# Optimization experiments

Hardware: AMD Instinct MI355X
Metric: run time of the kernel (lower is better)

## Reference

```python
import jax, jax.numpy as jnp
import numpy as np

N_BLOCKS = 8
HIDDEN = 256
BATCH = 4096
IN_DIM = 3 * N_BLOCKS


def setup_inputs() -> dict:
    key = jax.random.key(0)
    ks = jax.random.split(key, 32)
    s = 0.05
    d = {}
    d['x'] = jax.random.normal(ks[0], (BATCH, IN_DIM), dtype=jnp.float32)
    # per-block object encoders (stacked): in -> H, relu, H -> H, relu, H -> H
    d['o_W0'] = jax.random.normal(ks[1], (N_BLOCKS, IN_DIM, HIDDEN), dtype=jnp.float32) * s
    d['o_b0'] = jnp.zeros((N_BLOCKS, HIDDEN), jnp.float32)
    d['o_W1'] = jax.random.normal(ks[2], (N_BLOCKS, HIDDEN, HIDDEN), dtype=jnp.float32) * s
    d['o_b1'] = jnp.zeros((N_BLOCKS, HIDDEN), jnp.float32)
    d['o_W2'] = jax.random.normal(ks[3], (N_BLOCKS, HIDDEN, HIDDEN), dtype=jnp.float32) * s
    d['o_b2'] = jnp.zeros((N_BLOCKS, HIDDEN), jnp.float32)
    # clear predicate encoder: H -> H, relu, H -> H, relu, H -> 1, sigmoid
    d['c_W0'] = jax.random.normal(ks[4], (HIDDEN, HIDDEN), dtype=jnp.float32) * s
    d['c_b0'] = jnp.zeros((HIDDEN,), jnp.float32)
    d['c_W1'] = jax.random.normal(ks[5], (HIDDEN, HIDDEN), dtype=jnp.float32) * s
    d['c_b1'] = jnp.zeros((HIDDEN,), jnp.float32)
    d['c_W2'] = jax.random.normal(ks[6], (HIDDEN, 1), dtype=jnp.float32) * s
    d['c_b2'] = jnp.zeros((1,), jnp.float32)
    # ontable predicate encoder
    d['t_W0'] = jax.random.normal(ks[7], (HIDDEN, HIDDEN), dtype=jnp.float32) * s
    d['t_b0'] = jnp.zeros((HIDDEN,), jnp.float32)
    d['t_W1'] = jax.random.normal(ks[8], (HIDDEN, HIDDEN), dtype=jnp.float32) * s
    d['t_b1'] = jnp.zeros((HIDDEN,), jnp.float32)
    d['t_W2'] = jax.random.normal(ks[9], (HIDDEN, 1), dtype=jnp.float32) * s
    d['t_b2'] = jnp.zeros((1,), jnp.float32)
    # AonB predicate encoder: 2H -> H, relu, H -> H, relu, H -> 1, sigmoid
    d['a_W0'] = jax.random.normal(ks[10], (2 * HIDDEN, HIDDEN), dtype=jnp.float32) * s
    d['a_b0'] = jnp.zeros((HIDDEN,), jnp.float32)
    d['a_W1'] = jax.random.normal(ks[11], (HIDDEN, HIDDEN), dtype=jnp.float32) * s
    d['a_b1'] = jnp.zeros((HIDDEN,), jnp.float32)
    d['a_W2'] = jax.random.normal(ks[12], (HIDDEN, 1), dtype=jnp.float32) * s
    d['a_b2'] = jnp.zeros((1,), jnp.float32)
    return d


def _pred_mlp(h, W0, b0, W1, b1, W2, b2):
    h = jax.nn.relu(h @ W0 + b0)
    h = jax.nn.relu(h @ W1 + b1)
    return jax.nn.sigmoid(h @ W2 + b2)


def reference(x, o_W0, o_b0, o_W1, o_b1, o_W2, o_b2,
              c_W0, c_b0, c_W1, c_b1, c_W2, c_b2,
              t_W0, t_b0, t_W1, t_b1, t_W2, t_b2,
              a_W0, a_b0, a_W1, a_b1, a_W2, a_b2):
    B = x.shape[0]
    H = o_W0.shape[-1]
    # object encodings: (N, B, H), all N encoders batched via einsum
    h = jax.nn.relu(jnp.einsum('bd,ndh->nbh', x, o_W0) + o_b0[:, None, :])
    h = jax.nn.relu(jnp.einsum('nbh,nhk->nbk', h, o_W1) + o_b1[:, None, :])
    enc = jnp.einsum('nbh,nhk->nbk', h, o_W2) + o_b2[:, None, :]
    # clear/ontable predicates: (N, B, 1) -> (B, N)
    clear = _pred_mlp(enc, c_W0, c_b0, c_W1, c_b1, c_W2, c_b2)[..., 0].T
    table = _pred_mlp(enc, t_W0, t_b0, t_W1, t_b1, t_W2, t_b2)[..., 0].T
    # AonB over all pairs; split first layer to avoid materializing (N,N,B,2H)
    a_l = jnp.einsum('nbh,hk->nbk', enc, a_W0[:H])
    a_r = jnp.einsum('nbh,hk->nbk', enc, a_W0[H:])
    ph = jax.nn.relu(a_l[:, None] + a_r[None, :] + a_b0)  # (N, N, B, H), axis0=i(left), axis1=j(right)
    ph = jax.nn.relu(ph @ a_W1 + a_b1)
    aonb = jax.nn.sigmoid(ph @ a_W2 + a_b2)[..., 0]  # (N, N, B)
    aonb_b = jnp.transpose(aonb, (2, 0, 1))  # (B, N, N)
    # per block i: [AonB(i,0..N-1), clear(i), ontable(i)] concatenated over i
    out = jnp.concatenate([aonb_b, clear[..., None], table[..., None]], axis=2)
    return out.reshape(B, -1)
```

## Files before the change

### kernel.cpp

```cpp
#include <hip/hip_runtime.h>
#include <hip/hip_bf16.h>

#define OFF_O0   0u
#define OFF_O1   65536u
#define OFF_O2   589824u
#define OFF_C0   1114112u
#define OFF_C1   1179648u
#define OFF_T0   1245184u
#define OFF_T1   1310720u
#define OFF_AL   1376256u
#define OFF_AR   1441792u
#define OFF_A1   1507328u
#define OFF_ENC  1572864u
#define OFF_ALQ  9961472u
#define OFF_ARQ  18350080u

typedef short s8v __attribute__((ext_vector_type(8)));
typedef float f4v __attribute__((ext_vector_type(4)));

__device__ __forceinline__ unsigned short f2bf(float f) {
  unsigned u = __float_as_uint(f);
  unsigned r = (u + 0x7FFFu + ((u >> 16) & 1u)) >> 16;
  return (unsigned short)r;
}
__device__ __forceinline__ float bf2f(unsigned short h) {
  return __uint_as_float(((unsigned)h) << 16);
}

__device__ __forceinline__ void gemm_epilogue(
    f4v acc[4][4], const float* bias, int act,
    unsigned short* outb, unsigned short* gout)
{
  int lane = threadIdx.x & 63;
  int w    = threadIdx.x >> 6;
  int lr = lane & 15, kh = lane >> 4;
  if (outb) __syncthreads();
  #pragma unroll
  for (int nt = 0; nt < 4; nt++) {
    int col = w*64 + nt*16 + lr;
    float bv = bias ? bias[col] : 0.0f;
    #pragma unroll
    for (int mt = 0; mt < 4; mt++) {
      #pragma unroll
      for (int i = 0; i < 4; i++) {
        int row = mt*16 + kh*4 + i;
        float v = acc[mt][nt][i] + bv;
        if (act) v = fmaxf(v, 0.0f);
        unsigned short hh = f2bf(v);
        if (outb) {
          int bofs = (2*col) ^ ((row & 7) << 4);
          *(unsigned short*)((char*)outb + row*512 + bofs) = hh;
        }
        if (gout) gout[row*256 + col] = hh;
      }
    }
  }
  if (outb) __syncthreads();
}

__device__ __forceinline__ void gemm_core(
    const unsigned short* inb, const unsigned short* __restrict__ wt,
    f4v acc[4][4])
{
  int lane = threadIdx.x & 63;
  int w    = threadIdx.x >> 6;
  int lr = lane & 15, kh = lane >> 4;
  #pragma unroll
  for (int a = 0; a < 4; a++)
    #pragma unroll
    for (int b = 0; b < 4; b++) acc[a][b] = (f4v){0.f,0.f,0.f,0.f};
  #pragma unroll
  for (int k0 = 0; k0 < 256; k0 += 32) {
    s8v bfrag[4];
    #pragma unroll
    for (int nt = 0; nt < 4; nt++)
      bfrag[nt] = *(const s8v*)(wt + (w*64 + nt*16 + lr)*256 + k0 + kh*8);
    #pragma unroll
    for (int mt = 0; mt < 4; mt++) {
      int row = mt*16 + lr;
      int bofs = (2*k0 + kh*16) ^ ((row & 7) << 4);
      s8v afrag = *(const s8v*)((const char*)inb + row*512 + bofs);
      #pragma unroll
      for (int nt = 0; nt < 4; nt++)
        acc[mt][nt] = __builtin_amdgcn_mfma_f32_16x16x32_bf16(afrag, bfrag[nt], acc[mt][nt], 0, 0, 0);
    }
  }
}

__device__ __forceinline__ void gemm64(
    const unsigned short* inb, const unsigned short* __restrict__ wt,
    const float* bias, int act, unsigned short* outb, unsigned short* gout)
{
  f4v acc[4][4];
  gemm_core(inb, wt, acc);
  gemm_epilogue(acc, bias, act, outb, gout);
}

__device__ __forceinline__ void dot_tail(
    f4v acc[4][4], const float* __restrict__ bias,
    const float* __restrict__ w2, float b2,
    float* __restrict__ out, int m0, int offs, float* red)
{
  int lane = threadIdx.x & 63;
  int w    = threadIdx.x >> 6;
  int lr = lane & 15, kh = lane >> 4;
  float w2v[4], bv[4];
  #pragma unroll
  for (int nt = 0; nt < 4; nt++) {
    int col = w*64 + nt*16 + lr;
    w2v[nt] = w2[col];
    bv[nt]  = bias[col];
  }
  #pragma unroll
  for (int mt = 0; mt < 4; mt++) {
    #pragma unroll
    for (int i = 0; i < 4; i++) {
      float s = 0.0f;
      #pragma unroll
      for (int nt = 0; nt < 4; nt++)
        s += fmaxf(acc[mt][nt][i] + bv[nt], 0.0f) * w2v[nt];
      s += __shfl_xor(s, 1);
      s += __shfl_xor(s, 2);
      s += __shfl_xor(s, 4);
      s += __shfl_xor(s, 8);
      if (lr == 0) red[(mt*16 + kh*4 + i)*4 + w] = s;
    }
  }
  __syncthreads();
  if (threadIdx.x < 64) {
    int row = threadIdx.x;
    float s = red[row*4] + red[row*4+1] + red[row*4+2] + red[row*4+3];
    out[(m0 + row)*80 + offs] = 1.0f / (1.0f + __expf(-s - b2));
  }
}

__device__ __forceinline__ void gemm_x(
    const unsigned short* xb, const unsigned short* __restrict__ wt,
    const float* bias, unsigned short* outb)
{
  int lane = threadIdx.x & 63;
  int w    = threadIdx.x >> 6;
  int lr = lane & 15, kh = lane >> 4;
  f4v acc[4][4];
  #pragma unroll
  for (int a = 0; a < 4; a++)
    #pragma unroll
    for (int b = 0; b < 4; b++) acc[a][b] = (f4v){0.f,0.f,0.f,0.f};

  s8v bfrag[4];
  #pragma unroll
  for (int nt = 0; nt < 4; nt++)
    bfrag[nt] = *(const s8v*)(wt + (w*64 + nt*16 + lr)*32 + kh*8);
  #pragma unroll
  for (int mt = 0; mt < 4; mt++) {
    s8v afrag = *(const s8v*)(xb + (mt*16 + lr)*32 + kh*8);
    #pragma unroll
    for (int nt = 0; nt < 4; nt++)
      acc[mt][nt] = __builtin_amdgcn_mfma_f32_16x16x32_bf16(afrag, bfrag[nt], acc[mt][nt], 0, 0, 0);
  }
  gemm_epilogue(acc, bias, 1, outb, nullptr);
}

__global__ __launch_bounds__(256) void prep_kernel(
    const float* __restrict__ oW0, const float* __restrict__ oW1,
    const float* __restrict__ oW2, const float* __restrict__ cW0,
    const float* __restrict__ cW1, const float* __restrict__ tW0,
    const float* __restrict__ tW1, const float* __restrict__ aW0,
    const float* __restrict__ aW1, unsigned short* __restrict__ ws)
{
  __shared__ float t[32][33];
  int b = blockIdx.x;
  if (b < 1472) {
    int m = b >> 6, tile = b & 63;
    const float* src; unsigned short* dst;
    if      (m < 8)  { src = oW1 + m*65536;       dst = ws + OFF_O1 + m*65536; }
    else if (m < 16) { src = oW2 + (m-8)*65536;   dst = ws + OFF_O2 + (m-8)*65536; }
    else if (m == 16){ src = cW0;                 dst = ws + OFF_C0; }
    else if (m == 17){ src = cW1;                 dst = ws + OFF_C1; }
    else if (m == 18){ src = tW0;                 dst = ws + OFF_T0; }
    else if (m == 19){ src = tW1;                 dst = ws + OFF_T1; }
    else if (m == 20){ src = aW1;                 dst = ws + OFF_A1; }
    else if (m == 21){ src = aW0;                 dst = ws + OFF_AL; }
    else             { src = aW0 + 65536;         dst = ws + OFF_AR; }
    int kt = tile & 7, nt = tile >> 3;
    int tx = threadIdx.x & 31, ty = threadIdx.x >> 5;
    #pragma unroll
    for (int r = 0; r < 4; r++) {
      int ky = ty*4 + r;
      t[ky][tx] = src[(kt*32 + ky)*256 + nt*32 + tx];
    }
    __syncthreads();
    #pragma unroll
    for (int r = 0; r < 4; r++) {
      int ny = ty*4 + r;
      dst[(nt*32 + ny)*256 + kt*32 + tx] = f2bf(t[tx][ny]);
    }
  } else {
    int idx = (b - 1472)*256 + threadIdx.x;
    int k = idx & 31, n2 = (idx >> 5) & 255, nb = idx >> 13;
    float v = (k < 24) ? oW0[(nb*24 + k)*256 + n2] : 0.0f;
    ws[OFF_O0 + idx] = f2bf(v);
  }
}

__global__ __launch_bounds__(256) void encoder_kernel(
    const float* __restrict__ x,
    const float* __restrict__ ob0, const float* __restrict__ ob1,
    const float* __restrict__ ob2, const float* __restrict__ ab0,
    unsigned short* __restrict__ ws)
{
  __shared__ unsigned short buf[64*256];
  __shared__ unsigned short xb[64*32];
  int n  = blockIdx.x >> 6;
  int m0 = (blockIdx.x & 63) * 64;

  for (int t = threadIdx.x; t < 64*32; t += 256) {
    int row = t >> 5, c = t & 31;
    xb[t] = f2bf(c < 24 ? x[(m0 + row)*24 + c] : 0.0f);
  }
  __syncthreads();
  gemm_x (xb,  ws + OFF_O0 + n*8192,  ob0 + n*256, buf);
  gemm64 (buf, ws + OFF_O1 + n*65536, ob1 + n*256, 1, buf, nullptr);
  gemm64 (buf, ws + OFF_O2 + n*65536, ob2 + n*256, 0, buf,
          ws + OFF_ENC + (unsigned)(n*4096 + m0)*256);
  gemm64 (buf, ws + OFF_AL, nullptr, 0, nullptr,
          ws + OFF_ALQ + (unsigned)(n*4096 + m0)*256);
  gemm64 (buf, ws + OFF_AR, ab0, 0, nullptr,
          ws + OFF_ARQ + (unsigned)(n*4096 + m0)*256);
}

__global__ __launch_bounds__(512) void pair_kernel(
    const unsigned short* __restrict__ ws,
    const float* __restrict__ ab1, const float* __restrict__ aW2,
    const float* __restrict__ ab2, float* __restrict__ out)
{
  __shared__ unsigned short ph[2][64*256];
  __shared__ float red[2][256];
  int b = blockIdx.x;
  int i = b >> 6, chunk = b & 63;
  int m0 = chunk * 64;
  const unsigned short* Lp    = ws + OFF_ALQ + ((unsigned)i*4096u + m0)*256u;
  const unsigned short* Rbase = ws + OFF_ARQ + (unsigned)m0*256u;
  const unsigned short* wt    = ws + OFF_A1;

  int tid  = threadIdx.x;
  int lane = tid & 63, w = tid >> 6;
  int wm = w >> 2, wn = w & 3;
  int lr = lane & 15, kh = lane >> 4;

  int srow[4], sc8[4];
  #pragma unroll
  for (int q = 0; q < 4; q++) {
    int idx = q*512 + tid;
    srow[q] = idx >> 5; sc8[q] = idx & 31;
  }

  float w2v[4], bv[4];
  #pragma unroll
  for (int nt = 0; nt < 4; nt++) {
    int col = wn*64 + nt*16 + lr;
    w2v[nt] = aW2[col];
    bv[nt]  = ab1[col];
  }
  float b2 = ab2[0];

  #pragma unroll
  for (int q = 0; q < 4; q++) {
    unsigned off = (unsigned)srow[q]*256u + sc8[q]*8;
    s8v l8 = *(const s8v*)(Lp + off);
    s8v r8 = *(const s8v*)(Rbase + off);
    s8v o8;
    #pragma unroll
    for (int e = 0; e < 8; e++) {
      float v = bf2f((unsigned short)l8[e]) + bf2f((unsigned short)r8[e]);
      o8[e] = (short)f2bf(fmaxf(v, 0.0f));
    }
    *(s8v*)((char*)ph[0] + srow[q]*512 + ((sc8[q]*16) ^ ((srow[q] & 7) << 4))) = o8;
  }
  __syncthreads();

  int c = 0;
  for (int j = 0; j < 8; j++) {
    s8v Rr[4];
    if (j < 7) {
      const unsigned short* Rp = Rbase + (unsigned)(j+1)*(4096u*256u);
      #pragma unroll
      for (int q = 0; q < 4; q++)
        Rr[q] = *(const s8v*)(Rp + (unsigned)srow[q]*256u + sc8[q]*8);
    }
    f4v acc[2][4];
    #pragma unroll
    for (int a = 0; a < 2; a++)
      #pragma unroll
      for (int cc = 0; cc < 4; cc++) acc[a][cc] = (f4v){0.f,0.f,0.f,0.f};
    #pragma unroll
    for (int k0 = 0; k0 < 256; k0 += 32) {
      s8v bfrag[4];
      #pragma unroll
      for (int nt = 0; nt < 4; nt++)
        bfrag[nt] = *(const s8v*)(wt + (wn*64 + nt*16 + lr)*256 + k0 + kh*8);
      #pragma unroll
      for (int mt = 0; mt < 2; mt++) {
        int row = wm*32 + mt*16 + lr;
        int bofs = (2*k0 + kh*16) ^ ((row & 7) << 4);
        s8v afrag = *(const s8v*)((const char*)ph[c] + row*512 + bofs);
        #pragma unroll
        for (int nt = 0; nt < 4; nt++)
          acc[mt][nt] = __builtin_amdgcn_mfma_f32_16x16x32_bf16(afrag, bfrag[nt], acc[mt][nt], 0, 0, 0);
      }
    }
    if (j < 7) {
      #pragma unroll
      for (int q = 0; q < 4; q++) {
        s8v l8 = *(const s8v*)(Lp + (unsigned)srow[q]*256u + sc8[q]*8);
        s8v o8;
        #pragma unroll
        for (int e = 0; e < 8; e++) {
          float v = bf2f((unsigned short)l8[e]) + bf2f((unsigned short)Rr[q][e]);
          o8[e] = (short)f2bf(fmaxf(v, 0.0f));
        }
        *(s8v*)((char*)ph[c ^ 1] + srow[q]*512 + ((sc8[q]*16) ^ ((srow[q] & 7) << 4))) = o8;
      }
    }
    #pragma unroll
    for (int mt = 0; mt < 2; mt++) {
      #pragma unroll
      for (int ii = 0; ii < 4; ii++) {
        float s = 0.0f;
        #pragma unroll
        for (int nt = 0; nt < 4; nt++)
          s += fmaxf(acc[mt][nt][ii] + bv[nt], 0.0f) * w2v[nt];
        s += __shfl_xor(s, 1);
        s += __shfl_xor(s, 2);
        s += __shfl_xor(s, 4);
        s += __shfl_xor(s, 8);
        if (lr == 0) red[c][(wm*32 + mt*16 + kh*4 + ii)*4 + wn] = s;
      }
    }
    __syncthreads();
    if (tid < 64) {
      float s = red[c][tid*4] + red[c][tid*4+1] + red[c][tid*4+2] + red[c][tid*4+3];
      out[(m0 + tid)*80 + i*10 + j] = 1.0f / (1.0f + __expf(-s - b2));
    }
    c ^= 1;
  }
}

__global__ __launch_bounds__(256) void pred_kernel(
    const unsigned short* __restrict__ ws,
    const float* __restrict__ cb0, const float* __restrict__ cb1,
    const float* __restrict__ cW2, const float* __restrict__ cb2,
    const float* __restrict__ tb0, const float* __restrict__ tb1,
    const float* __restrict__ tW2, const float* __restrict__ tb2,
    float* __restrict__ out)
{
  __shared__ unsigned short bufA[64*256];
  __shared__ float red[256];
  int b  = blockIdx.x;
  int p  = b >> 9;
  int n  = (b >> 6) & 7;
  int m0 = (b & 63) * 64;
  const unsigned short* encp = ws + OFF_ENC + (unsigned)(n*4096 + m0)*256;
  for (int t = threadIdx.x; t < 64*32; t += 256) {
    int row = t >> 5, chunk = t & 31;
    s8v v = *(const s8v*)(encp + row*256 + chunk*8);
    int bofs = (chunk*16) ^ ((row & 7) << 4);
    *(s8v*)((char*)bufA + row*512 + bofs) = v;
  }
  __syncthreads();
  const unsigned short* W0 = ws + (p ? OFF_T0 : OFF_C0);
  const unsigned short* W1 = ws + (p ? OFF_T1 : OFF_C1);
  gemm64(bufA, W0, p ? tb0 : cb0, 1, bufA, nullptr);
  f4v acc[4][4];
  gemm_core(bufA, W1, acc);
  dot_tail(acc, p ? tb1 : cb1, p ? tW2 : cW2,
           p ? tb2[0] : cb2[0], out, m0, n*10 + 8 + p, red);
}

extern "C" void kernel_launch(void* const* d_in, const int* in_sizes, int n_in,
                              void* d_out, int out_size, void* d_ws, size_t ws_size,
                              hipStream_t stream) {
  (void)in_sizes; (void)n_in; (void)out_size; (void)ws_size;
  const float* x   = (const float*)d_in[0];
  const float* oW0 = (const float*)d_in[1];
  const float* ob0 = (const float*)d_in[2];
  const float* oW1 = (const float*)d_in[3];
  const float* ob1 = (const float*)d_in[4];
  const float* oW2 = (const float*)d_in[5];
  const float* ob2 = (const float*)d_in[6];
  const float* cW0 = (const float*)d_in[7];
  const float* cb0 = (const float*)d_in[8];
  const float* cW1 = (const float*)d_in[9];
  const float* cb1 = (const float*)d_in[10];
  const float* cW2 = (const float*)d_in[11];
  const float* cb2 = (const float*)d_in[12];
  const float* tW0 = (const float*)d_in[13];
  const float* tb0 = (const float*)d_in[14];
  const float* tW1 = (const float*)d_in[15];
  const float* tb1 = (const float*)d_in[16];
  const float* tW2 = (const float*)d_in[17];
  const float* tb2 = (const float*)d_in[18];
  const float* aW0 = (const float*)d_in[19];
  const float* ab0 = (const float*)d_in[20];
  const float* aW1 = (const float*)d_in[21];
  const float* ab1 = (const float*)d_in[22];
  const float* aW2 = (const float*)d_in[23];
  const float* ab2 = (const float*)d_in[24];
  unsigned short* ws = (unsigned short*)d_ws;
  float* out = (float*)d_out;

  hipLaunchKernelGGL(prep_kernel, dim3(1728), dim3(256), 0, stream,
                     oW0, oW1, oW2, cW0, cW1, tW0, tW1, aW0, aW1, ws);
  hipLaunchKernelGGL(encoder_kernel, dim3(512), dim3(256), 0, stream,
                     x, ob0, ob1, ob2, ab0, ws);
  hipLaunchKernelGGL(pair_kernel, dim3(512), dim3(512), 0, stream,
                     ws, ab1, aW2, ab2, out);
  hipLaunchKernelGGL(pred_kernel, dim3(1024), dim3(256), 0, stream,
                     ws, cb0, cb1, cW2, cb2, tb0, tb1, tW2, tb2, out);
}
```

Baseline: 181.8 us.

## Merge pair and predicate kernels into one heterogeneous tail kernel

Fuses the AonB pair kernel and the clear/ontable predicate kernel into a single launch of 1536 blocks of 512 threads. Pair and predicate blocks are interleaved by block index. The predicate path is rewritten for 8 waves with 2x4 tiles and double LDS buffers instead of 4 waves. This removes one launch and its tail bubble and lets the lighter predicate blocks fill idle CUs while pair blocks run. The cost is higher LDS and register usage for predicate blocks, which may lower occupancy.

```diff
diff --git a/kernel.cpp b/kernel.cpp
--- a/kernel.cpp
+++ b/kernel.cpp
@@ -94,44 +94,6 @@
   f4v acc[4][4];
   gemm_core(inb, wt, acc);
   gemm_epilogue(acc, bias, act, outb, gout);
-}
-
-__device__ __forceinline__ void dot_tail(
-    f4v acc[4][4], const float* __restrict__ bias,
-    const float* __restrict__ w2, float b2,
-    float* __restrict__ out, int m0, int offs, float* red)
-{
-  int lane = threadIdx.x & 63;
-  int w    = threadIdx.x >> 6;
-  int lr = lane & 15, kh = lane >> 4;
-  float w2v[4], bv[4];
-  #pragma unroll
-  for (int nt = 0; nt < 4; nt++) {
-    int col = w*64 + nt*16 + lr;
-    w2v[nt] = w2[col];
-    bv[nt]  = bias[col];
-  }
-  #pragma unroll
-  for (int mt = 0; mt < 4; mt++) {
-    #pragma unroll
-    for (int i = 0; i < 4; i++) {
-      float s = 0.0f;
-      #pragma unroll
-      for (int nt = 0; nt < 4; nt++)
-        s += fmaxf(acc[mt][nt][i] + bv[nt], 0.0f) * w2v[nt];
-      s += __shfl_xor(s, 1);
-      s += __shfl_xor(s, 2);
-      s += __shfl_xor(s, 4);
-      s += __shfl_xor(s, 8);
-      if (lr == 0) red[(mt*16 + kh*4 + i)*4 + w] = s;
-    }
-  }
-  __syncthreads();
-  if (threadIdx.x < 64) {
-    int row = threadIdx.x;
-    float s = red[row*4] + red[row*4+1] + red[row*4+2] + red[row*4+3];
-    out[(m0 + row)*80 + offs] = 1.0f / (1.0f + __expf(-s - b2));
-  }
 }
 
 __device__ __forceinline__ void gemm_x(
@@ -229,152 +191,243 @@
           ws + OFF_ARQ + (unsigned)(n*4096 + m0)*256);
 }
 
-__global__ __launch_bounds__(512) void pair_kernel(
+__global__ __launch_bounds__(512) void tail_kernel(
     const unsigned short* __restrict__ ws,
     const float* __restrict__ ab1, const float* __restrict__ aW2,
-    const float* __restrict__ ab2, float* __restrict__ out)
-{
-  __shared__ unsigned short ph[2][64*256];
-  __shared__ float red[2][256];
-  int b = blockIdx.x;
-  int i = b >> 6, chunk = b & 63;
-  int m0 = chunk * 64;
-  const unsigned short* Lp    = ws + OFF_ALQ + ((unsigned)i*4096u + m0)*256u;
-  const unsigned short* Rbase = ws + OFF_ARQ + (unsigned)m0*256u;
-  const unsigned short* wt    = ws + OFF_A1;
-
-  int tid  = threadIdx.x;
-  int lane = tid & 63, w = tid >> 6;
-  int wm = w >> 2, wn = w & 3;
-  int lr = lane & 15, kh = lane >> 4;
-
-  int srow[4], sc8[4];
-  #pragma unroll
-  for (int q = 0; q < 4; q++) {
-    int idx = q*512 + tid;
-    srow[q] = idx >> 5; sc8[q] = idx & 31;
-  }
-
-  float w2v[4], bv[4];
-  #pragma unroll
-  for (int nt = 0; nt < 4; nt++) {
-    int col = wn*64 + nt*16 + lr;
-    w2v[nt] = aW2[col];
-    bv[nt]  = ab1[col];
-  }
-  float b2 = ab2[0];
-
-  #pragma unroll
-  for (int q = 0; q < 4; q++) {
-    unsigned off = (unsigned)srow[q]*256u + sc8[q]*8;
-    s8v l8 = *(const s8v*)(Lp + off);
-    s8v r8 = *(const s8v*)(Rbase + off);
-    s8v o8;
-    #pragma unroll
-    for (int e = 0; e < 8; e++) {
-      float v = bf2f((unsigned short)l8[e]) + bf2f((unsigned short)r8[e]);
-      o8[e] = (short)f2bf(fmaxf(v, 0.0f));
-    }
-    *(s8v*)((char*)ph[0] + srow[q]*512 + ((sc8[q]*16) ^ ((srow[q] & 7) << 4))) = o8;
-  }
-  __syncthreads();
-
-  int c = 0;
-  for (int j = 0; j < 8; j++) {
-    s8v Rr[4];
-    if (j < 7) {
-      const unsigned short* Rp = Rbase + (unsigned)(j+1)*(4096u*256u);
-      #pragma unroll
-      for (int q = 0; q < 4; q++)
-        Rr[q] = *(const s8v*)(Rp + (unsigned)srow[q]*256u + sc8[q]*8);
-    }
-    f4v acc[2][4];
-    #pragma unroll
-    for (int a = 0; a < 2; a++)
-      #pragma unroll
-      for (int cc = 0; cc < 4; cc++) acc[a][cc] = (f4v){0.f,0.f,0.f,0.f};
-    #pragma unroll
-    for (int k0 = 0; k0 < 256; k0 += 32) {
-      s8v bfrag[4];
-      #pragma unroll
-      for (int nt = 0; nt < 4; nt++)
-        bfrag[nt] = *(const s8v*)(wt + (wn*64 + nt*16 + lr)*256 + k0 + kh*8);
-      #pragma unroll
-      for (int mt = 0; mt < 2; mt++) {
-        int row = wm*32 + mt*16 + lr;
-        int bofs = (2*k0 + kh*16) ^ ((row & 7) << 4);
-        s8v afrag = *(const s8v*)((const char*)ph[c] + row*512 + bofs);
-        #pragma unroll
-        for (int nt = 0; nt < 4; nt++)
-          acc[mt][nt] = __builtin_amdgcn_mfma_f32_16x16x32_bf16(afrag, bfrag[nt], acc[mt][nt], 0, 0, 0);
-      }
-    }
-    if (j < 7) {
-      #pragma unroll
-      for (int q = 0; q < 4; q++) {
-        s8v l8 = *(const s8v*)(Lp + (unsigned)srow[q]*256u + sc8[q]*8);
-        s8v o8;
-        #pragma unroll
-        for (int e = 0; e < 8; e++) {
-          float v = bf2f((unsigned short)l8[e]) + bf2f((unsigned short)Rr[q][e]);
-          o8[e] = (short)f2bf(fmaxf(v, 0.0f));
-        }
-        *(s8v*)((char*)ph[c ^ 1] + srow[q]*512 + ((sc8[q]*16) ^ ((srow[q] & 7) << 4))) = o8;
-      }
-    }
-    #pragma unroll
-    for (int mt = 0; mt < 2; mt++) {
-      #pragma unroll
-      for (int ii = 0; ii < 4; ii++) {
-        float s = 0.0f;
-        #pragma unroll
-        for (int nt = 0; nt < 4; nt++)
-          s += fmaxf(acc[mt][nt][ii] + bv[nt], 0.0f) * w2v[nt];
-        s += __shfl_xor(s, 1);
-        s += __shfl_xor(s, 2);
-        s += __shfl_xor(s, 4);
-        s += __shfl_xor(s, 8);
-        if (lr == 0) red[c][(wm*32 + mt*16 + kh*4 + ii)*4 + wn] = s;
-      }
-    }
-    __syncthreads();
-    if (tid < 64) {
-      float s = red[c][tid*4] + red[c][tid*4+1] + red[c][tid*4+2] + red[c][tid*4+3];
-      out[(m0 + tid)*80 + i*10 + j] = 1.0f / (1.0f + __expf(-s - b2));
-    }
-    c ^= 1;
-  }
-}
-
-__global__ __launch_bounds__(256) void pred_kernel(
-    const unsigned short* __restrict__ ws,
+    const float* __restrict__ ab2,
     const float* __restrict__ cb0, const float* __restrict__ cb1,
     const float* __restrict__ cW2, const float* __restrict__ cb2,
     const float* __restrict__ tb0, const float* __restrict__ tb1,
     const float* __restrict__ tW2, const float* __restrict__ tb2,
     float* __restrict__ out)
 {
-  __shared__ unsigned short bufA[64*256];
-  __shared__ float red[256];
-  int b  = blockIdx.x;
-  int p  = b >> 9;
-  int n  = (b >> 6) & 7;
-  int m0 = (b & 63) * 64;
-  const unsigned short* encp = ws + OFF_ENC + (unsigned)(n*4096 + m0)*256;
-  for (int t = threadIdx.x; t < 64*32; t += 256) {
-    int row = t >> 5, chunk = t & 31;
-    s8v v = *(const s8v*)(encp + row*256 + chunk*8);
-    int bofs = (chunk*16) ^ ((row & 7) << 4);
-    *(s8v*)((char*)bufA + row*512 + bofs) = v;
-  }
-  __syncthreads();
-  const unsigned short* W0 = ws + (p ? OFF_T0 : OFF_C0);
-  const unsigned short* W1 = ws + (p ? OFF_T1 : OFF_C1);
-  gemm64(bufA, W0, p ? tb0 : cb0, 1, bufA, nullptr);
-  f4v acc[4][4];
-  gemm_core(bufA, W1, acc);
-  dot_tail(acc, p ? tb1 : cb1, p ? tW2 : cW2,
-           p ? tb2[0] : cb2[0], out, m0, n*10 + 8 + p, red);
+  __shared__ unsigned short bufU[2][64*256];
+  __shared__ float redU[2][256];
+  int b = blockIdx.x;
+  int is_pair, id;
+  if (b < 1024) { is_pair = ((b & 1) == 0); id = b >> 1; }
+  else          { is_pair = 0;              id = b - 512; }
+
+  int tid  = threadIdx.x;
+  int lane = tid & 63, w = tid >> 6;
+  int wm = w >> 2, wn = w & 3;
+  int lr = lane & 15, kh = lane >> 4;
+
+  if (is_pair) {
+    int i = id >> 6, chunk = id & 63;
+    int m0 = chunk * 64;
+    const unsigned short* Lp    = ws + OFF_ALQ + ((unsigned)i*4096u + m0)*256u;
+    const unsigned short* Rbase = ws + OFF_ARQ + (unsigned)m0*256u;
+    const unsigned short* wt    = ws + OFF_A1;
+
+    int srow[4], sc8[4];
+    #pragma unroll
+    for (int q = 0; q < 4; q++) {
+      int idx = q*512 + tid;
+      srow[q] = idx >> 5; sc8[q] = idx & 31;
+    }
+
+    float w2v[4], bv[4];
+    #pragma unroll
+    for (int nt = 0; nt < 4; nt++) {
+      int col = wn*64 + nt*16 + lr;
+      w2v[nt] = aW2[col];
+      bv[nt]  = ab1[col];
+    }
+    float b2 = ab2[0];
+
+    #pragma unroll
+    for (int q = 0; q < 4; q++) {
+      unsigned off = (unsigned)srow[q]*256u + sc8[q]*8;
+      s8v l8 = *(const s8v*)(Lp + off);
+      s8v r8 = *(const s8v*)(Rbase + off);
+      s8v o8;
+      #pragma unroll
+      for (int e = 0; e < 8; e++) {
+        float v = bf2f((unsigned short)l8[e]) + bf2f((unsigned short)r8[e]);
+        o8[e] = (short)f2bf(fmaxf(v, 0.0f));
+      }
+      *(s8v*)((char*)bufU[0] + srow[q]*512 + ((sc8[q]*16) ^ ((srow[q] & 7) << 4))) = o8;
+    }
+    __syncthreads();
+
+    int c = 0;
+    for (int j = 0; j < 8; j++) {
+      s8v Rr[4];
+      if (j < 7) {
+        const unsigned short* Rp = Rbase + (unsigned)(j+1)*(4096u*256u);
+        #pragma unroll
+        for (int q = 0; q < 4; q++)
+          Rr[q] = *(const s8v*)(Rp + (unsigned)srow[q]*256u + sc8[q]*8);
+      }
+      f4v acc[2][4];
+      #pragma unroll
+      for (int a = 0; a < 2; a++)
+        #pragma unroll
+        for (int cc = 0; cc < 4; cc++) acc[a][cc] = (f4v){0.f,0.f,0.f,0.f};
+      #pragma unroll
+      for (int k0 = 0; k0 < 256; k0 += 32) {
+        s8v bfrag[4];
+        #pragma unroll
+        for (int nt = 0; nt < 4; nt++)
+          bfrag[nt] = *(const s8v*)(wt + (wn*64 + nt*16 + lr)*256 + k0 + kh*8);
+        #pragma unroll
+        for (int mt = 0; mt < 2; mt++) {
+          int row = wm*32 + mt*16 + lr;
+          int bofs = (2*k0 + kh*16) ^ ((row & 7) << 4);
+          s8v afrag = *(const s8v*)((const char*)bufU[c] + row*512 + bofs);
+          #pragma unroll
+          for (int nt = 0; nt < 4; nt++)
+            acc[mt][nt] = __builtin_amdgcn_mfma_f32_16x16x32_bf16(afrag, bfrag[nt], acc[mt][nt], 0, 0, 0);
+        }
+      }
+      if (j < 7) {
+        #pragma unroll
+        for (int q = 0; q < 4; q++) {
+          s8v l8 = *(const s8v*)(Lp + (unsigned)srow[q]*256u + sc8[q]*8);
+          s8v o8;
+          #pragma unroll
+          for (int e = 0; e < 8; e++) {
+            float v = bf2f((unsigned short)l8[e]) + bf2f((unsigned short)Rr[q][e]);
+            o8[e] = (short)f2bf(fmaxf(v, 0.0f));
+          }
+          *(s8v*)((char*)bufU[c ^ 1] + srow[q]*512 + ((sc8[q]*16) ^ ((srow[q] & 7) << 4))) = o8;
+        }
+      }
+      #pragma unroll
+      for (int mt = 0; mt < 2; mt++) {
+        #pragma unroll
+        for (int ii = 0; ii < 4; ii++) {
+          float s = 0.0f;
+          #pragma unroll
+          for (int nt = 0; nt < 4; nt++)
+            s += fmaxf(acc[mt][nt][ii] + bv[nt], 0.0f) * w2v[nt];
+          s += __shfl_xor(s, 1);
+          s += __shfl_xor(s, 2);
+          s += __shfl_xor(s, 4);
+          s += __shfl_xor(s, 8);
+          if (lr == 0) redU[c][(wm*32 + mt*16 + kh*4 + ii)*4 + wn] = s;
+        }
+      }
+      __syncthreads();
+      if (tid < 64) {
+        float s = redU[c][tid*4] + redU[c][tid*4+1] + redU[c][tid*4+2] + redU[c][tid*4+3];
+        out[(m0 + tid)*80 + i*10 + j] = 1.0f / (1.0f + __expf(-s - b2));
+      }
+      c ^= 1;
+    }
+  } else {
+    int p  = id >> 9;
+    int n  = (id >> 6) & 7;
+    int m0 = (id & 63) * 64;
+    const unsigned short* encp = ws + OFF_ENC + (unsigned)(n*4096 + m0)*256;
+
+    #pragma unroll
+    for (int q = 0; q < 4; q++) {
+      int idx = q*512 + tid;
+      int row = idx >> 5, c8 = idx & 31;
+      s8v v = *(const s8v*)(encp + (unsigned)row*256u + c8*8);
+      *(s8v*)((char*)bufU[0] + row*512 + ((c8*16) ^ ((row & 7) << 4))) = v;
+    }
+    __syncthreads();
+
+    const unsigned short* W0 = ws + (p ? OFF_T0 : OFF_C0);
+    const unsigned short* W1 = ws + (p ? OFF_T1 : OFF_C1);
+    const float* b0 = p ? tb0 : cb0;
+    const float* b1 = p ? tb1 : cb1;
+    const float* w2 = p ? tW2 : cW2;
+    float b2s = p ? tb2[0] : cb2[0];
+
+    {
+      f4v acc[2][4];
+      #pragma unroll
+      for (int a = 0; a < 2; a++)
+        #pragma unroll
+        for (int cc = 0; cc < 4; cc++) acc[a][cc] = (f4v){0.f,0.f,0.f,0.f};
+      #pragma unroll
+      for (int k0 = 0; k0 < 256; k0 += 32) {
+        s8v bfrag[4];
+        #pragma unroll
+        for (int nt = 0; nt < 4; nt++)
+          bfrag[nt] = *(const s8v*)(W0 + (wn*64 + nt*16 + lr)*256 + k0 + kh*8);
+        #pragma unroll
+        for (int mt = 0; mt < 2; mt++) {
+          int row = wm*32 + mt*16 + lr;
+          int bofs = (2*k0 + kh*16) ^ ((row & 7) << 4);
+          s8v afrag = *(const s8v*)((const char*)bufU[0] + row*512 + bofs);
+          #pragma unroll
+          for (int nt = 0; nt < 4; nt++)
+            acc[mt][nt] = __builtin_amdgcn_mfma_f32_16x16x32_bf16(afrag, bfrag[nt], acc[mt][nt], 0, 0, 0);
+        }
+      }
+      #pragma unroll
+      for (int nt = 0; nt < 4; nt++) {
+        int col = wn*64 + nt*16 + lr;
+        float bv = b0[col];
+        #pragma unroll
+        for (int mt = 0; mt < 2; mt++) {
+          #pragma unroll
+          for (int ii = 0; ii < 4; ii++) {
+            int row = wm*32 + mt*16 + kh*4 + ii;
+            unsigned short hh = f2bf(fmaxf(acc[mt][nt][ii] + bv, 0.0f));
+            *(unsigned short*)((char*)bufU[1] + row*512 + ((2*col) ^ ((row & 7) << 4))) = hh;
+          }
+        }
+      }
+    }
+    __syncthreads();
+
+    {
+      float w2v[4], bv[4];
+      #pragma unroll
+      for (int nt = 0; nt < 4; nt++) {
+        int col = wn*64 + nt*16 + lr;
+        w2v[nt] = w2[col];
+        bv[nt]  = b1[col];
+      }
+      f4v acc[2][4];
+      #pragma unroll
+      for (int a = 0; a < 2; a++)
+        #pragma unroll
+        for (int cc = 0; cc < 4; cc++) acc[a][cc] = (f4v){0.f,0.f,0.f,0.f};
+      #pragma unroll
+      for (int k0 = 0; k0 < 256; k0 += 32) {
+        s8v bfrag[4];
+        #pragma unroll
+        for (int nt = 0; nt < 4; nt++)
+          bfrag[nt] = *(const s8v*)(W1 + (wn*64 + nt*16 + lr)*256 + k0 + kh*8);
+        #pragma unroll
+        for (int mt = 0; mt < 2; mt++) {
+          int row = wm*32 + mt*16 + lr;
+          int bofs = (2*k0 + kh*16) ^ ((row & 7) << 4);
+          s8v afrag = *(const s8v*)((const char*)bufU[1] + row*512 + bofs);
+          #pragma unroll
+          for (int nt = 0; nt < 4; nt++)
+            acc[mt][nt] = __builtin_amdgcn_mfma_f32_16x16x32_bf16(afrag, bfrag[nt], acc[mt][nt], 0, 0, 0);
+        }
+      }
+      #pragma unroll
+      for (int mt = 0; mt < 2; mt++) {
+        #pragma unroll
+        for (int ii = 0; ii < 4; ii++) {
+          float s = 0.0f;
+          #pragma unroll
+          for (int nt = 0; nt < 4; nt++)
+            s += fmaxf(acc[mt][nt][ii] + bv[nt], 0.0f) * w2v[nt];
+          s += __shfl_xor(s, 1);
+          s += __shfl_xor(s, 2);
+          s += __shfl_xor(s, 4);
+          s += __shfl_xor(s, 8);
+          if (lr == 0) redU[0][(wm*32 + mt*16 + kh*4 + ii)*4 + wn] = s;
+        }
+      }
+      __syncthreads();
+      if (tid < 64) {
+        float s = redU[0][tid*4] + redU[0][tid*4+1] + redU[0][tid*4+2] + redU[0][tid*4+3];
+        out[(m0 + tid)*80 + n*10 + 8 + p] = 1.0f / (1.0f + __expf(-s - b2s));
+      }
+    }
+  }
 }
 
 extern "C" void kernel_launch(void* const* d_in, const int* in_sizes, int n_in,
@@ -413,8 +466,7 @@
                      oW0, oW1, oW2, cW0, cW1, tW0, tW1, aW0, aW1, ws);
   hipLaunchKernelGGL(encoder_kernel, dim3(512), dim3(256), 0, stream,
                      x, ob0, ob1, ob2, ab0, ws);
-  hipLaunchKernelGGL(pair_kernel, dim3(512), dim3(512), 0, stream,
-                     ws, ab1, aW2, ab2, out);
-  hipLaunchKernelGGL(pred_kernel, dim3(1024), dim3(256), 0, stream,
-                     ws, cb0, cb1, cW2, cb2, tb0, tb1, tW2, tb2, out);
-}
+  hipLaunchKernelGGL(tail_kernel, dim3(1536), dim3(512), 0, stream,
+                     ws, ab1, aW2, ab2, cb0, cb1, cW2, cb2,
+                     tb0, tb1, tW2, tb2, out);
+}
```

Result: slower. 245.9 us (+35.3%).

## Store AonB projections in MFMA fragment layout and build pair tiles in registers

Applied to the files above, without the earlier changes.

The encoder now writes the left/right AonB projections in a pre-swizzled MFMA A-fragment layout through a shared staging buffer. The pair kernel then loads each lane's fragment straight from global memory, computes relu(L+R) in registers and feeds it to the MFMA, with no LDS tile, double buffer or per-j sync for the pair activations. This removes LDS traffic and shared-memory usage in the hot pair kernel, which may raise occupancy. In exchange every k-step issues global loads, so latency must be hidden by the cache and occupancy, and the encoder epilogue gains extra syncs.

```diff
diff --git a/kernel.cpp b/kernel.cpp
--- a/kernel.cpp
+++ b/kernel.cpp
@@ -159,6 +159,43 @@
       acc[mt][nt] = __builtin_amdgcn_mfma_f32_16x16x32_bf16(afrag, bfrag[nt], acc[mt][nt], 0, 0, 0);
   }
   gemm_epilogue(acc, bias, 1, outb, nullptr);
+}
+
+__device__ __forceinline__ void epi_frag(
+    f4v acc[4][4], const float* bias, unsigned short* fb,
+    unsigned short* __restrict__ gdst)
+{
+  int lane = threadIdx.x & 63;
+  int w    = threadIdx.x >> 6;
+  int lr = lane & 15, kh = lane >> 4;
+  #pragma unroll
+  for (int half = 0; half < 2; half++) {
+    __syncthreads();
+    #pragma unroll
+    for (int nt = 0; nt < 4; nt++) {
+      int col = w*64 + nt*16 + lr;
+      float bv = bias ? bias[col] : 0.0f;
+      int k0   = w*2 + (nt >> 1);
+      int lsub = ((nt & 1)*2 + (lr >> 3))*16;
+      int eb   = lr & 7;
+      #pragma unroll
+      for (int mt2 = 0; mt2 < 2; mt2++) {
+        int mt = half*2 + mt2;
+        #pragma unroll
+        for (int i = 0; i < 4; i++) {
+          float v = acc[mt][nt][i] + bv;
+          fb[mt2*4096 + k0*512 + (kh*4 + i + lsub)*8 + eb] = f2bf(v);
+        }
+      }
+    }
+    __syncthreads();
+    unsigned short* g = gdst + half*2*4096;
+    #pragma unroll
+    for (int t = 0; t < 4; t++) {
+      int idx = t*256 + threadIdx.x;
+      *(s8v*)(g + idx*8) = *(const s8v*)(fb + idx*8);
+    }
+  }
 }
 
 __global__ __launch_bounds__(256) void prep_kernel(
@@ -211,6 +248,7 @@
 {
   __shared__ unsigned short buf[64*256];
   __shared__ unsigned short xb[64*32];
+  __shared__ __align__(16) unsigned short fb[8192];
   int n  = blockIdx.x >> 6;
   int m0 = (blockIdx.x & 63) * 64;
 
@@ -223,10 +261,17 @@
   gemm64 (buf, ws + OFF_O1 + n*65536, ob1 + n*256, 1, buf, nullptr);
   gemm64 (buf, ws + OFF_O2 + n*65536, ob2 + n*256, 0, buf,
           ws + OFF_ENC + (unsigned)(n*4096 + m0)*256);
-  gemm64 (buf, ws + OFF_AL, nullptr, 0, nullptr,
-          ws + OFF_ALQ + (unsigned)(n*4096 + m0)*256);
-  gemm64 (buf, ws + OFF_AR, ab0, 0, nullptr,
-          ws + OFF_ARQ + (unsigned)(n*4096 + m0)*256);
+  unsigned fbase = (unsigned)n*1048576u + (unsigned)(m0 >> 4)*4096u;
+  {
+    f4v acc[4][4];
+    gemm_core(buf, ws + OFF_AL, acc);
+    epi_frag(acc, nullptr, fb, ws + OFF_ALQ + fbase);
+  }
+  {
+    f4v acc[4][4];
+    gemm_core(buf, ws + OFF_AR, acc);
+    epi_frag(acc, ab0, fb, ws + OFF_ARQ + fbase);
+  }
 }
 
 __global__ __launch_bounds__(512) void pair_kernel(
@@ -234,26 +279,19 @@
     const float* __restrict__ ab1, const float* __restrict__ aW2,
     const float* __restrict__ ab2, float* __restrict__ out)
 {
-  __shared__ unsigned short ph[2][64*256];
   __shared__ float red[2][256];
   int b = blockIdx.x;
   int i = b >> 6, chunk = b & 63;
   int m0 = chunk * 64;
-  const unsigned short* Lp    = ws + OFF_ALQ + ((unsigned)i*4096u + m0)*256u;
-  const unsigned short* Rbase = ws + OFF_ARQ + (unsigned)m0*256u;
-  const unsigned short* wt    = ws + OFF_A1;
+  const unsigned short* Lf  = ws + OFF_ALQ + (unsigned)i*1048576u
+                              + (unsigned)(m0 >> 4)*4096u;
+  const unsigned short* Rf0 = ws + OFF_ARQ + (unsigned)(m0 >> 4)*4096u;
+  const unsigned short* wt  = ws + OFF_A1;
 
   int tid  = threadIdx.x;
   int lane = tid & 63, w = tid >> 6;
   int wm = w >> 2, wn = w & 3;
   int lr = lane & 15, kh = lane >> 4;
-
-  int srow[4], sc8[4];
-  #pragma unroll
-  for (int q = 0; q < 4; q++) {
-    int idx = q*512 + tid;
-    srow[q] = idx >> 5; sc8[q] = idx & 31;
-  }
 
   float w2v[4], bv[4];
   #pragma unroll
@@ -264,64 +302,38 @@
   }
   float b2 = ab2[0];
 
-  #pragma unroll
-  for (int q = 0; q < 4; q++) {
-    unsigned off = (unsigned)srow[q]*256u + sc8[q]*8;
-    s8v l8 = *(const s8v*)(Lp + off);
-    s8v r8 = *(const s8v*)(Rbase + off);
-    s8v o8;
-    #pragma unroll
-    for (int e = 0; e < 8; e++) {
-      float v = bf2f((unsigned short)l8[e]) + bf2f((unsigned short)r8[e]);
-      o8[e] = (short)f2bf(fmaxf(v, 0.0f));
-    }
-    *(s8v*)((char*)ph[0] + srow[q]*512 + ((sc8[q]*16) ^ ((srow[q] & 7) << 4))) = o8;
-  }
-  __syncthreads();
-
-  int c = 0;
   for (int j = 0; j < 8; j++) {
-    s8v Rr[4];
-    if (j < 7) {
-      const unsigned short* Rp = Rbase + (unsigned)(j+1)*(4096u*256u);
-      #pragma unroll
-      for (int q = 0; q < 4; q++)
-        Rr[q] = *(const s8v*)(Rp + (unsigned)srow[q]*256u + sc8[q]*8);
-    }
+    const unsigned short* Rf = Rf0 + (unsigned)j*1048576u;
     f4v acc[2][4];
     #pragma unroll
     for (int a = 0; a < 2; a++)
       #pragma unroll
       for (int cc = 0; cc < 4; cc++) acc[a][cc] = (f4v){0.f,0.f,0.f,0.f};
-    #pragma unroll
-    for (int k0 = 0; k0 < 256; k0 += 32) {
+
+    #pragma unroll
+    for (int k0 = 0; k0 < 8; k0++) {
       s8v bfrag[4];
       #pragma unroll
       for (int nt = 0; nt < 4; nt++)
-        bfrag[nt] = *(const s8v*)(wt + (wn*64 + nt*16 + lr)*256 + k0 + kh*8);
+        bfrag[nt] = *(const s8v*)(wt + (wn*64 + nt*16 + lr)*256 + k0*32 + kh*8);
       #pragma unroll
       for (int mt = 0; mt < 2; mt++) {
-        int row = wm*32 + mt*16 + lr;
-        int bofs = (2*k0 + kh*16) ^ ((row & 7) << 4);
-        s8v afrag = *(const s8v*)((const char*)ph[c] + row*512 + bofs);
+        int rt = wm*2 + mt;
+        unsigned fo = (unsigned)(rt*8 + k0)*512u + (unsigned)lane*8u;
+        s8v l8 = *(const s8v*)(Lf + fo);
+        s8v r8 = *(const s8v*)(Rf + fo);
+        s8v a8;
+        #pragma unroll
+        for (int e = 0; e < 8; e++) {
+          float v = bf2f((unsigned short)l8[e]) + bf2f((unsigned short)r8[e]);
+          a8[e] = (short)f2bf(fmaxf(v, 0.0f));
+        }
         #pragma unroll
         for (int nt = 0; nt < 4; nt++)
-          acc[mt][nt] = __builtin_amdgcn_mfma_f32_16x16x32_bf16(afrag, bfrag[nt], acc[mt][nt], 0, 0, 0);
+          acc[mt][nt] = __builtin_amdgcn_mfma_f32_16x16x32_bf16(a8, bfrag[nt], acc[mt][nt], 0, 0, 0);
       }
     }
-    if (j < 7) {
-      #pragma unroll
-      for (int q = 0; q < 4; q++) {
-        s8v l8 = *(const s8v*)(Lp + (unsigned)srow[q]*256u + sc8[q]*8);
-        s8v o8;
-        #pragma unroll
-        for (int e = 0; e < 8; e++) {
-          float v = bf2f((unsigned short)l8[e]) + bf2f((unsigned short)Rr[q][e]);
-          o8[e] = (short)f2bf(fmaxf(v, 0.0f));
-        }
-        *(s8v*)((char*)ph[c ^ 1] + srow[q]*512 + ((sc8[q]*16) ^ ((srow[q] & 7) << 4))) = o8;
-      }
-    }
+    int c = j & 1;
     #pragma unroll
     for (int mt = 0; mt < 2; mt++) {
       #pragma unroll
@@ -342,7 +354,6 @@
       float s = red[c][tid*4] + red[c][tid*4+1] + red[c][tid*4+2] + red[c][tid*4+3];
       out[(m0 + tid)*80 + i*10 + j] = 1.0f / (1.0f + __expf(-s - b2));
     }
-    c ^= 1;
   }
 }
 
```

Result: slower. 265.8 us (+46.2%).
